# Kernel optimization log

Measured on AMD Instinct MI355X. Metric: run time of the kernel, lower is better.

## Reference

```python
import jax, jax.numpy as jnp
import numpy as np

B, S, X, Y = 32, 3, 512, 512  # batch, O(3) spin components, lattice X, lattice Y

_L_np = np.array([[[0, 0, 0], [0, 0, -1], [0, 1, 0]],
                  [[0, 0, 1], [0, 0, 0], [-1, 0, 0]],
                  [[0, -1, 0], [1, 0, 0], [0, 0, 0]]], dtype=np.float32)


def setup_inputs() -> dict:
    key = jax.random.key(0)
    k_s, = jax.random.split(key, 1)
    s = jax.random.normal(k_s, (B, S, X, Y), dtype=jnp.float32)
    t = jnp.ones((), dtype=jnp.float32)
    C0 = jnp.ones((), dtype=jnp.float32)  # cc=[1.0] learnable coefficient
    L = jnp.asarray(_L_np)                # fixed SO(3) generators [s, r, a]
    return {"s": s, "t": t, "C0": C0, "L": L}


def reference(s, t, C0, L):
    # Psi0.grad: F = sum_mu (roll(s,+1,mu) + roll(s,-1,mu)); nearest-neighbor stencil
    Fn = (jnp.roll(s, 1, axis=2) + jnp.roll(s, -1, axis=2)
          + jnp.roll(s, 1, axis=3) + jnp.roll(s, -1, axis=3))
    # Lsig = -einsum('bsxy,sra->braxy', s, L); out = einsum('bsaxy,bsxy->baxy', Lsig, Fn)
    # fused: out[b,a,x,y] = -sum_{s,r} s[b,s,x,y] * L[s,r,a] * Fn[b,r,x,y]
    F = -jnp.einsum('bsxy,sra,brxy->baxy', s, L, Fn)
    # Coeff(t): cc=[1.0], EvenOdd=True, single coeff => Coeff(t) = C0 (t-independent)
    coeff = C0
    return coeff * F
```

## Files before the change

kernel.cpp:

```cpp
#include <hip/hip_runtime.h>


constexpr int B = 32, X = 512, Y = 512;
constexpr int XY = X * Y;

__global__ __launch_bounds__(256)
void psi0_kernel(const float* __restrict__ s,
                 const float* __restrict__ C0p,
                 const float* __restrict__ Lp,
                 float* __restrict__ out)
{
    const int tid  = threadIdx.x;
    const int lane = tid & 63;
    const int wv   = tid >> 6;
    const int bid  = blockIdx.x;
    const int b    = bid >> 7;
    const int x    = ((bid & 127) << 2) + wv;
    const int y0   = lane << 3;

    const int xm = (x == 0)     ? X - 1 : x - 1;
    const int xp = (x == X - 1) ? 0     : x + 1;

    const float C0 = C0p[0];
    const float cA0 = -C0 * Lp[15];
    const float cB0 = -C0 * Lp[21];
    const float cA1 = -C0 * Lp[7];
    const float cB1 = -C0 * Lp[19];
    const float cA2 = -C0 * Lp[5];
    const float cB2 = -C0 * Lp[11];

    const size_t baseB = (size_t)b * 3 * XY;
    const size_t offC  = (size_t)x  * Y + y0;
    const size_t offU  = (size_t)xm * Y + y0;
    const size_t offD  = (size_t)xp * Y + y0;

    float sc[3][8];
    float Fn[3][8];

    #pragma unroll
    for (int c = 0; c < 3; ++c) {
        const float* p = s + baseB + (size_t)c * XY;
        const float4 c0 = *(const float4*)(p + offC);
        const float4 c1 = *(const float4*)(p + offC + 4);
        const float4 u0 = *(const float4*)(p + offU);
        const float4 u1 = *(const float4*)(p + offU + 4);
        const float4 d0 = *(const float4*)(p + offD);
        const float4 d1 = *(const float4*)(p + offD + 4);

        const float lf = __shfl(c1.w, (lane + 63) & 63, 64);
        const float rt = __shfl(c0.x, (lane + 1) & 63, 64);

        sc[c][0] = c0.x; sc[c][1] = c0.y; sc[c][2] = c0.z; sc[c][3] = c0.w;
        sc[c][4] = c1.x; sc[c][5] = c1.y; sc[c][6] = c1.z; sc[c][7] = c1.w;

        Fn[c][0] = u0.x + d0.x + lf   + c0.y;
        Fn[c][1] = u0.y + d0.y + c0.x + c0.z;
        Fn[c][2] = u0.z + d0.z + c0.y + c0.w;
        Fn[c][3] = u0.w + d0.w + c0.z + c1.x;
        Fn[c][4] = u1.x + d1.x + c0.w + c1.y;
        Fn[c][5] = u1.y + d1.y + c1.x + c1.z;
        Fn[c][6] = u1.z + d1.z + c1.y + c1.w;
        Fn[c][7] = u1.w + d1.w + c1.z + rt;
    }

    float o[3][8];
    #pragma unroll
    for (int e = 0; e < 8; ++e) {
        o[0][e] = cA0 * (sc[1][e] * Fn[2][e]) + cB0 * (sc[2][e] * Fn[1][e]);
        o[1][e] = cA1 * (sc[0][e] * Fn[2][e]) + cB1 * (sc[2][e] * Fn[0][e]);
        o[2][e] = cA2 * (sc[0][e] * Fn[1][e]) + cB2 * (sc[1][e] * Fn[0][e]);
    }

    #pragma unroll
    for (int a = 0; a < 3; ++a) {
        float* q = out + baseB + (size_t)a * XY + offC;
        *(float4*)(q)     = make_float4(o[a][0], o[a][1], o[a][2], o[a][3]);
        *(float4*)(q + 4) = make_float4(o[a][4], o[a][5], o[a][6], o[a][7]);
    }
}

extern "C" void kernel_launch(void* const* d_in, const int* in_sizes, int n_in,
                              void* d_out, int out_size, void* d_ws, size_t ws_size,
                              hipStream_t stream)
{
    const float* s   = (const float*)d_in[0];
    const float* C0p = (const float*)d_in[2];
    const float* Lp  = (const float*)d_in[3];
    float* out = (float*)d_out;

    const int blocks = B * (X / 4);
    psi0_kernel<<<blocks, 256, 0, stream>>>(s, C0p, Lp, out);
}
```

Measured before the change: 185.8 us.

## Process four rows per wave with rolling register reuse and XCD-aware block mapping

Each wave now computes four consecutive x-rows and keeps a sliding window of loaded rows in registers, so each input row is loaded about 1.5 times instead of three. Block ids are permuted so that neighbouring slabs are distributed across XCD groups. Fewer blocks are launched, each doing more work. This adds register pressure and lowers the number of waves in flight, which could reduce latency hiding.

```diff
diff --git a/kernel.cpp b/kernel.cpp
--- a/kernel.cpp
+++ b/kernel.cpp
@@ -4,49 +4,31 @@
 constexpr int B = 32, X = 512, Y = 512;
 constexpr int XY = X * Y;
 
-__global__ __launch_bounds__(256)
-void psi0_kernel(const float* __restrict__ s,
-                 const float* __restrict__ C0p,
-                 const float* __restrict__ Lp,
-                 float* __restrict__ out)
+struct RowC { float4 lo, hi; };
+struct Row3 { RowC c[3]; };
+
+__device__ __forceinline__ void load_row(const float* __restrict__ sb, size_t rowoff, Row3& r)
 {
-    const int tid  = threadIdx.x;
-    const int lane = tid & 63;
-    const int wv   = tid >> 6;
-    const int bid  = blockIdx.x;
-    const int b    = bid >> 7;
-    const int x    = ((bid & 127) << 2) + wv;
-    const int y0   = lane << 3;
-
-    const int xm = (x == 0)     ? X - 1 : x - 1;
-    const int xp = (x == X - 1) ? 0     : x + 1;
-
-    const float C0 = C0p[0];
-    const float cA0 = -C0 * Lp[15];
-    const float cB0 = -C0 * Lp[21];
-    const float cA1 = -C0 * Lp[7];
-    const float cB1 = -C0 * Lp[19];
-    const float cA2 = -C0 * Lp[5];
-    const float cB2 = -C0 * Lp[11];
-
-    const size_t baseB = (size_t)b * 3 * XY;
-    const size_t offC  = (size_t)x  * Y + y0;
-    const size_t offU  = (size_t)xm * Y + y0;
-    const size_t offD  = (size_t)xp * Y + y0;
-
-    float sc[3][8];
-    float Fn[3][8];
-
     #pragma unroll
     for (int c = 0; c < 3; ++c) {
-        const float* p = s + baseB + (size_t)c * XY;
-        const float4 c0 = *(const float4*)(p + offC);
-        const float4 c1 = *(const float4*)(p + offC + 4);
-        const float4 u0 = *(const float4*)(p + offU);
-        const float4 u1 = *(const float4*)(p + offU + 4);
-        const float4 d0 = *(const float4*)(p + offD);
-        const float4 d1 = *(const float4*)(p + offD + 4);
+        const float* p = sb + (size_t)c * XY + rowoff;
+        r.c[c].lo = *(const float4*)(p);
+        r.c[c].hi = *(const float4*)(p + 4);
+    }
+}
 
+__device__ __forceinline__ void compute_store(const Row3& U, const Row3& Cn, const Row3& Dn,
+                                              float* __restrict__ ob, size_t rowoff, int lane,
+                                              float cA0, float cB0, float cA1,
+                                              float cB1, float cA2, float cB2)
+{
+    float Fn[3][8];
+    float sc[3][8];
+    #pragma unroll
+    for (int c = 0; c < 3; ++c) {
+        const float4 c0 = Cn.c[c].lo, c1 = Cn.c[c].hi;
+        const float4 u0 = U.c[c].lo,  u1 = U.c[c].hi;
+        const float4 d0 = Dn.c[c].lo, d1 = Dn.c[c].hi;
         const float lf = __shfl(c1.w, (lane + 63) & 63, 64);
         const float rt = __shfl(c0.x, (lane + 1) & 63, 64);
 
@@ -73,10 +55,58 @@
 
     #pragma unroll
     for (int a = 0; a < 3; ++a) {
-        float* q = out + baseB + (size_t)a * XY + offC;
+        float* q = ob + (size_t)a * XY + rowoff;
         *(float4*)(q)     = make_float4(o[a][0], o[a][1], o[a][2], o[a][3]);
         *(float4*)(q + 4) = make_float4(o[a][4], o[a][5], o[a][6], o[a][7]);
     }
+}
+
+__global__ __launch_bounds__(256)
+void psi0_kernel(const float* __restrict__ s,
+                 const float* __restrict__ C0p,
+                 const float* __restrict__ Lp,
+                 float* __restrict__ out)
+{
+    const int tid  = threadIdx.x;
+    const int lane = tid & 63;
+    const int wv   = tid >> 6;
+
+    const int bid = blockIdx.x;
+    const int g   = (bid & 7) * 128 + (bid >> 3);
+
+    const int b    = g >> 5;
+    const int slab = g & 31;
+    const int x0   = slab * 16 + wv * 4;
+    const int y0   = lane << 3;
+
+    const float C0 = C0p[0];
+    const float cA0 = -C0 * Lp[15];
+    const float cB0 = -C0 * Lp[21];
+    const float cA1 = -C0 * Lp[7];
+    const float cB1 = -C0 * Lp[19];
+    const float cA2 = -C0 * Lp[5];
+    const float cB2 = -C0 * Lp[11];
+
+    const float* sb = s   + (size_t)b * 3 * XY + y0;
+    float*       ob = out + (size_t)b * 3 * XY + y0;
+
+    auto roff = [](int x) { return (size_t)((x + X) & (X - 1)) * Y; };
+
+    Row3 Ar, Br, Cr, Dr;
+    load_row(sb, roff(x0 - 1), Ar);
+    load_row(sb, roff(x0),     Br);
+    load_row(sb, roff(x0 + 1), Cr);
+    load_row(sb, roff(x0 + 2), Dr);
+
+    compute_store(Ar, Br, Cr, ob, (size_t)x0 * Y, lane, cA0, cB0, cA1, cB1, cA2, cB2);
+    load_row(sb, roff(x0 + 3), Ar);
+
+    compute_store(Br, Cr, Dr, ob, (size_t)(x0 + 1) * Y, lane, cA0, cB0, cA1, cB1, cA2, cB2);
+    load_row(sb, roff(x0 + 4), Br);
+
+    compute_store(Cr, Dr, Ar, ob, (size_t)(x0 + 2) * Y, lane, cA0, cB0, cA1, cB1, cA2, cB2);
+
+    compute_store(Dr, Ar, Br, ob, (size_t)(x0 + 3) * Y, lane, cA0, cB0, cA1, cB1, cA2, cB2);
 }
 
 extern "C" void kernel_launch(void* const* d_in, const int* in_sizes, int n_in,
@@ -88,6 +118,6 @@
     const float* Lp  = (const float*)d_in[3];
     float* out = (float*)d_out;
 
-    const int blocks = B * (X / 4);
+    const int blocks = B * (X / 16);
     psi0_kernel<<<blocks, 256, 0, stream>>>(s, C0p, Lp, out);
 }
```

Result: slower. 198.3 us (+6.7%).

## Stage 10-row halo tile in LDS with direct global-to-LDS loads and nontemporal stores

Applied to the files above, without the earlier changes.

Each block now handles 8 rows of one batch. It stages the 10 halo rows of all three components in shared memory, using global_load_lds when the builtin exists, and computes the stencil from LDS. The aim is to cut redundant global reads of the up and down neighbour rows, since the old kernel read each row three times. Block indices are also remapped across groups of 8, and outputs use nontemporal stores. In exchange the block uses about 60KB of LDS, which limits occupancy, and the load phase does not overlap with compute.

```diff
diff --git a/kernel.cpp b/kernel.cpp
--- a/kernel.cpp
+++ b/kernel.cpp
@@ -3,6 +3,16 @@
 
 constexpr int B = 32, X = 512, Y = 512;
 constexpr int XY = X * Y;
+constexpr int R  = 8;
+constexpr int HR = R + 2;
+
+typedef float f32x4 __attribute__((ext_vector_type(4)));
+
+__device__ __forceinline__ void nt_store4(float* p, float a, float b, float c, float d)
+{
+    f32x4 v = { a, b, c, d };
+    __builtin_nontemporal_store(v, (f32x4*)p);
+}
 
 __global__ __launch_bounds__(256)
 void psi0_kernel(const float* __restrict__ s,
@@ -10,18 +20,46 @@
                  const float* __restrict__ Lp,
                  float* __restrict__ out)
 {
+    __shared__ __align__(16) float lds[HR][3][Y];
+
     const int tid  = threadIdx.x;
     const int lane = tid & 63;
     const int wv   = tid >> 6;
-    const int bid  = blockIdx.x;
-    const int b    = bid >> 7;
-    const int x    = ((bid & 127) << 2) + wv;
-    const int y0   = lane << 3;
 
-    const int xm = (x == 0)     ? X - 1 : x - 1;
-    const int xp = (x == X - 1) ? 0     : x + 1;
+    const int bid = blockIdx.x;
+    const int g   = (bid & 7) * 256 + (bid >> 3);
+    const int b   = g >> 6;
+    const int x0  = (g & 63) * R;
 
-    const float C0 = C0p[0];
+    const size_t base = (size_t)b * 3 * XY;
+
+#if __has_builtin(__builtin_amdgcn_global_load_lds)
+    for (int rc = wv; rc < HR * 3; rc += 4) {
+        const int r = rc / 3, c = rc % 3;
+        const int xr = (x0 + r - 1 + X) & (X - 1);
+        const float* gp = s + base + (size_t)c * XY + (size_t)xr * Y;
+        #pragma unroll
+        for (int j = 0; j < 2; ++j) {
+            __builtin_amdgcn_global_load_lds(
+                (const __attribute__((address_space(1))) void*)(gp + j * 256 + lane * 4),
+                (__attribute__((address_space(3))) void*)(&lds[r][c][j * 256]),
+                16, 0, 0);
+        }
+    }
+    asm volatile("s_waitcnt vmcnt(0)" ::: "memory");
+#else
+    for (int v = tid; v < HR * 3 * (Y / 4); v += 256) {
+        const int rc = v >> 7;
+        const int yy = (v & 127) << 2;
+        const int r = rc / 3, c = rc % 3;
+        const int xr = (x0 + r - 1 + X) & (X - 1);
+        *(f32x4*)&lds[r][c][yy] =
+            *(const f32x4*)(s + base + (size_t)c * XY + (size_t)xr * Y + yy);
+    }
+#endif
+    __syncthreads();
+
+    const float C0  = C0p[0];
     const float cA0 = -C0 * Lp[15];
     const float cB0 = -C0 * Lp[21];
     const float cA1 = -C0 * Lp[7];
@@ -29,53 +67,42 @@
     const float cA2 = -C0 * Lp[5];
     const float cB2 = -C0 * Lp[11];
 
-    const size_t baseB = (size_t)b * 3 * XY;
-    const size_t offC  = (size_t)x  * Y + y0;
-    const size_t offU  = (size_t)xm * Y + y0;
-    const size_t offD  = (size_t)xp * Y + y0;
+    #pragma unroll
+    for (int p = 0; p < 4; ++p) {
+        const int ro = (p << 1) + (tid >> 7);
+        const int y0 = (tid & 127) << 2;
+        const int ym = (y0 - 1) & (Y - 1);
+        const int yp = (y0 + 4) & (Y - 1);
 
-    float sc[3][8];
-    float Fn[3][8];
+        float sc[3][4], Fn[3][4];
+        #pragma unroll
+        for (int c = 0; c < 3; ++c) {
+            const float* lc = &lds[ro + 1][c][0];
+            const f32x4 cc = *(const f32x4*)(lc + y0);
+            const f32x4 uu = *(const f32x4*)(&lds[ro][c][y0]);
+            const f32x4 dd = *(const f32x4*)(&lds[ro + 2][c][y0]);
+            const float lf = lc[ym];
+            const float rt = lc[yp];
 
-    #pragma unroll
-    for (int c = 0; c < 3; ++c) {
-        const float* p = s + baseB + (size_t)c * XY;
-        const float4 c0 = *(const float4*)(p + offC);
-        const float4 c1 = *(const float4*)(p + offC + 4);
-        const float4 u0 = *(const float4*)(p + offU);
-        const float4 u1 = *(const float4*)(p + offU + 4);
-        const float4 d0 = *(const float4*)(p + offD);
-        const float4 d1 = *(const float4*)(p + offD + 4);
+            sc[c][0] = cc.x; sc[c][1] = cc.y; sc[c][2] = cc.z; sc[c][3] = cc.w;
+            Fn[c][0] = uu.x + dd.x + lf   + cc.y;
+            Fn[c][1] = uu.y + dd.y + cc.x + cc.z;
+            Fn[c][2] = uu.z + dd.z + cc.y + cc.w;
+            Fn[c][3] = uu.w + dd.w + cc.z + rt;
+        }
 
-        const float lf = __shfl(c1.w, (lane + 63) & 63, 64);
-        const float rt = __shfl(c0.x, (lane + 1) & 63, 64);
+        float o0[4], o1[4], o2[4];
+        #pragma unroll
+        for (int e = 0; e < 4; ++e) {
+            o0[e] = cA0 * (sc[1][e] * Fn[2][e]) + cB0 * (sc[2][e] * Fn[1][e]);
+            o1[e] = cA1 * (sc[0][e] * Fn[2][e]) + cB1 * (sc[2][e] * Fn[0][e]);
+            o2[e] = cA2 * (sc[0][e] * Fn[1][e]) + cB2 * (sc[1][e] * Fn[0][e]);
+        }
 
-        sc[c][0] = c0.x; sc[c][1] = c0.y; sc[c][2] = c0.z; sc[c][3] = c0.w;
-        sc[c][4] = c1.x; sc[c][5] = c1.y; sc[c][6] = c1.z; sc[c][7] = c1.w;
-
-        Fn[c][0] = u0.x + d0.x + lf   + c0.y;
-        Fn[c][1] = u0.y + d0.y + c0.x + c0.z;
-        Fn[c][2] = u0.z + d0.z + c0.y + c0.w;
-        Fn[c][3] = u0.w + d0.w + c0.z + c1.x;
-        Fn[c][4] = u1.x + d1.x + c0.w + c1.y;
-        Fn[c][5] = u1.y + d1.y + c1.x + c1.z;
-        Fn[c][6] = u1.z + d1.z + c1.y + c1.w;
-        Fn[c][7] = u1.w + d1.w + c1.z + rt;
-    }
-
-    float o[3][8];
-    #pragma unroll
-    for (int e = 0; e < 8; ++e) {
-        o[0][e] = cA0 * (sc[1][e] * Fn[2][e]) + cB0 * (sc[2][e] * Fn[1][e]);
-        o[1][e] = cA1 * (sc[0][e] * Fn[2][e]) + cB1 * (sc[2][e] * Fn[0][e]);
-        o[2][e] = cA2 * (sc[0][e] * Fn[1][e]) + cB2 * (sc[1][e] * Fn[0][e]);
-    }
-
-    #pragma unroll
-    for (int a = 0; a < 3; ++a) {
-        float* q = out + baseB + (size_t)a * XY + offC;
-        *(float4*)(q)     = make_float4(o[a][0], o[a][1], o[a][2], o[a][3]);
-        *(float4*)(q + 4) = make_float4(o[a][4], o[a][5], o[a][6], o[a][7]);
+        const size_t ro_off = (size_t)(x0 + ro) * Y + y0;
+        nt_store4(out + base + 0 * (size_t)XY + ro_off, o0[0], o0[1], o0[2], o0[3]);
+        nt_store4(out + base + 1 * (size_t)XY + ro_off, o1[0], o1[1], o1[2], o1[3]);
+        nt_store4(out + base + 2 * (size_t)XY + ro_off, o2[0], o2[1], o2[2], o2[3]);
     }
 }
 
@@ -88,6 +115,6 @@
     const float* Lp  = (const float*)d_in[3];
     float* out = (float*)d_out;
 
-    const int blocks = B * (X / 4);
+    const int blocks = B * (X / R);
     psi0_kernel<<<blocks, 256, 0, stream>>>(s, C0p, Lp, out);
 }
```

Result: no change. 183.1 us (-1.4%).
